# Kernel optimization log

Measured on AMD Instinct MI355X. Metric: run time of the kernel, lower is better.

The kernel has to match this reference:

```python
import jax, jax.numpy as jnp
import numpy as np

B, H, S, DH = 8, 16, 512, 64
HID = H * DH


def setup_inputs() -> dict:
    key = jax.random.key(0)
    ks = jax.random.split(key, 16)
    # padding vectors: 1s up to a per-sample valid length, 0s afterwards
    # (first zero index == valid length, matching create_padding_matrix semantics)
    len_q = jax.random.randint(ks[0], (B,), S // 2, S + 1)
    len_k = jax.random.randint(ks[1], (B,), S // 2, S + 1)
    r = jnp.arange(S)
    pq = (r[None, :] < len_q[:, None]).astype(jnp.int32)
    pk = (r[None, :] < len_k[:, None]).astype(jnp.int32)
    sc = 0.02
    inp = {
        "padding_vector_q": pq,
        "padding_vector_k": pk,
        "query_t_1": jnp.zeros((1,), jnp.float32),
        "key_t": jnp.zeros((1,), jnp.float32),
        "hidden_states": jnp.zeros((1,), jnp.float32),
        "hidden_states_t_1": jnp.zeros((1,), jnp.float32),
        "hidden_from_last": jax.random.normal(ks[2], (B, H, S, DH), jnp.float32),
        "hidden_current": jax.random.normal(ks[3], (B, H, S, DH), jnp.float32),
        "max_n_codes": S,
        "interpretabity": 0,
        "iter_idx": 0,
        "W_v1": jax.random.normal(ks[4], (HID, HID), jnp.float32) * sc,
        "b_v1": jnp.zeros((HID,), jnp.float32),
        "W_v": jax.random.normal(ks[5], (HID, HID), jnp.float32) * sc,
        "b_v": jnp.zeros((HID,), jnp.float32),
        "W_q": jax.random.normal(ks[6], (HID, HID), jnp.float32) * sc,
        "b_q": jnp.zeros((HID,), jnp.float32),
        "W_k": jax.random.normal(ks[7], (HID, HID), jnp.float32) * sc,
        "b_k": jnp.zeros((HID,), jnp.float32),
        "W_cat": jax.random.normal(ks[8], (2 * DH, DH), jnp.float32) * sc,
        "b_cat": jnp.zeros((DH,), jnp.float32),
    }
    return inp


def reference(padding_vector_q, padding_vector_k, query_t_1, key_t,
              hidden_states, hidden_states_t_1, hidden_from_last, hidden_current,
              max_n_codes, interpretabity, iter_idx,
              W_v1, b_v1, W_v, b_v, W_q, b_q, W_k, b_k, W_cat, b_cat):
    b, h, s, dh = hidden_from_last.shape
    hid = h * dh
    # permute(0,2,1,3).flatten(start_dim=2): [B,H,S,Dh] -> [B,S,H*Dh]
    flat_last = hidden_from_last.transpose(0, 2, 1, 3).reshape(b, s, hid)
    flat_cur = hidden_current.transpose(0, 2, 1, 3).reshape(b, s, hid)

    def heads(x):  # [B,S,HID] -> [B,H,S,Dh]
        return x.reshape(b, s, h, dh).transpose(0, 2, 1, 3)

    v1 = heads(flat_last @ W_v1 + b_v1)   # value_t_1(hidden_from_last)
    vt = heads(flat_cur @ W_v + b_v)      # value(hidden_current)
    q = heads(flat_last @ W_q + b_q)
    k = heads(flat_cur @ W_k + b_k)

    scores = jnp.einsum('bhqd,bhkd->bhqk', q, k) / jnp.sqrt(jnp.float32(dh))
    scores_t = scores.transpose(0, 1, 3, 2)  # [B,H,Sk,Sq] (original permute(0,1,3,2))

    # vectorized per-sample padding mask: valid window [0:padd_q, 0:padd_k]
    def first_zero(v):
        hz = jnp.any(v == 0, axis=1)
        return jnp.where(hz, jnp.argmax(v == 0, axis=1), s)

    pq_len = first_zero(padding_vector_q)
    pk_len = first_zero(padding_vector_k)
    r = jnp.arange(s)
    valid = (r[None, :, None] < pq_len[:, None, None]) & \
            (r[None, None, :] < pk_len[:, None, None])  # [B,S,S]
    mask = (~valid)[:, None, :, :]  # True = masked, broadcast over heads

    # -1e9 underflows to exactly 0 after softmax in fp32, matching the
    # masked_fill(-inf) -> softmax -> masked_fill(0) chain without NaN rows
    NEG = jnp.float32(-1e9)
    attn = jax.nn.softmax(jnp.where(mask, NEG, scores_t), axis=-1)
    attention_values = jnp.where(mask, jnp.float32(0), attn)

    context_layer = jnp.einsum('bhks,bhsd->bhkd', attention_values, v1)
    context_layer2 = jnp.concatenate([context_layer, vt], axis=-1) @ W_cat + b_cat
    return attention_values, scores_t, context_layer2, context_layer
```

## Files before the change

### kernel.cpp

```cpp
#include <hip/hip_runtime.h>
#include <cstddef>

#define NB 8
#define NH 16
#define NS 512
#define NDH 64
#define NHID 1024
#define NBH (NB*NH)

#define QKV_ELEMS (NB*NH*NS*NDH)
#define ATTN_ELEMS ((size_t)NB*NH*(size_t)NS*NS)

typedef __bf16 bf16;
typedef __attribute__((ext_vector_type(8))) __bf16 bf16x8;
typedef __attribute__((ext_vector_type(4))) __bf16 bf16x4;
typedef __attribute__((ext_vector_type(4))) float f32x4;
typedef unsigned int u32;

__device__ __forceinline__ void gload_lds16(const void* g, void* l) {
    __builtin_amdgcn_global_load_lds(
        (const __attribute__((address_space(1))) u32*)g,
        (__attribute__((address_space(3))) u32*)l, 16, 0, 0);
}

__device__ __forceinline__ int swz(int idx, int row) { return idx ^ ((row & 7) << 3); }

__global__ void lens_kernel(const int* __restrict__ pq, const int* __restrict__ pk,
                            int* __restrict__ lens) {
    int bi = blockIdx.x;
    const int* v = (bi < NB) ? pq : pk;
    int b = bi & (NB - 1);
    int lane = threadIdx.x;
    int local = NS;
#pragma unroll
    for (int p = 0; p < NS / 64; ++p) {
        int idx = p * 64 + lane;
        if (v[b * NS + idx] == 0 && idx < local) local = idx;
    }
#pragma unroll
    for (int m = 32; m >= 1; m >>= 1) {
        int o = __shfl_xor(local, m, 64);
        local = min(local, o);
    }
    if (lane == 0) lens[bi] = local;
}

__global__ __launch_bounds__(256) void cvtA_kernel(
    const float* __restrict__ hl, const float* __restrict__ hc,
    bf16* __restrict__ al, bf16* __restrict__ ac) {
    const float* src = blockIdx.z ? hc : hl;
    bf16* dst = blockIdx.z ? ac : al;
    int tid = blockIdx.x * 256 + threadIdx.x;
    int d8 = tid & 7, s = (tid >> 3) & 511, h = (tid >> 12) & 15, b = tid >> 16;
    const float* p = &src[(((size_t)b * NH + h) * NS + s) * NDH + d8 * 8];
    float4 v0 = *(const float4*)p;
    float4 v1 = *(const float4*)(p + 4);
    bf16x8 o;
    o[0] = (bf16)v0.x; o[1] = (bf16)v0.y; o[2] = (bf16)v0.z; o[3] = (bf16)v0.w;
    o[4] = (bf16)v1.x; o[5] = (bf16)v1.y; o[6] = (bf16)v1.z; o[7] = (bf16)v1.w;
    *(bf16x8*)&dst[((size_t)(b * NS + s)) * NHID + h * NDH + d8 * 8] = o;
}

__global__ __launch_bounds__(256) void cvtW_kernel(
    const float* __restrict__ Wq, const float* __restrict__ Wk,
    const float* __restrict__ Wv1, const float* __restrict__ Wv,
    bf16* __restrict__ Wt) {
    const float* W;
    switch (blockIdx.z) {
        case 0: W = Wq; break;
        case 1: W = Wk; break;
        case 2: W = Wv1; break;
        default: W = Wv; break;
    }
    bf16* out = Wt + (size_t)blockIdx.z * NHID * NHID;
    __shared__ bf16 T[64][72];
    int t = threadIdx.x;
    int k0 = blockIdx.y * 64, n0 = blockIdx.x * 64;
#pragma unroll
    for (int p = 0; p < 4; ++p) {
        int kk = p * 16 + (t >> 4), c4 = (t & 15) * 4;
        float4 v = *(const float4*)&W[(size_t)(k0 + kk) * NHID + n0 + c4];
        T[c4 + 0][kk] = (bf16)v.x;
        T[c4 + 1][kk] = (bf16)v.y;
        T[c4 + 2][kk] = (bf16)v.z;
        T[c4 + 3][kk] = (bf16)v.w;
    }
    __syncthreads();
#pragma unroll
    for (int p = 0; p < 2; ++p) {
        int f = p * 256 + t;
        int nn = f >> 3, k8 = (f & 7) * 8;
        bf16x8 o;
#pragma unroll
        for (int e = 0; e < 8; ++e) o[e] = T[nn][k8 + e];
        *(bf16x8*)&out[(size_t)(n0 + nn) * NHID + k0 + k8] = o;
    }
}

__global__ __launch_bounds__(256) void proj_kernel(
    const bf16* __restrict__ al, const bf16* __restrict__ ac,
    const bf16* __restrict__ Wt,
    const float* __restrict__ bq, const float* __restrict__ bk,
    const float* __restrict__ bv1, const float* __restrict__ bv,
    bf16* __restrict__ oq, bf16* __restrict__ ok,
    bf16* __restrict__ ov1, bf16* __restrict__ ovt) {
    __shared__ bf16 As[128 * 64];
    __shared__ bf16 Bs[128 * 64];
    const bf16* A; const bf16* W; const float* bias; bf16* dst;
    switch (blockIdx.z) {
        case 0: A = al; W = Wt;                 bias = bq;  dst = oq;  break;
        case 1: A = ac; W = Wt + 1048576;       bias = bk;  dst = ok;  break;
        case 2: A = al; W = Wt + 2097152;       bias = bv1; dst = ov1; break;
        default: A = ac; W = Wt + 3145728;      bias = bv;  dst = ovt; break;
    }
    int t = threadIdx.x, lane = t & 63, w = t >> 6;
    int wm = w & 1, wn = w >> 1;
    int m0 = blockIdx.y * 128, n0 = blockIdx.x * 128;
    int lrow = lane >> 3, lk8 = (lane & 7) * 8;
    f32x4 acc[4][4];
#pragma unroll
    for (int i = 0; i < 4; ++i)
#pragma unroll
        for (int j = 0; j < 4; ++j) acc[i][j] = (f32x4){0.f, 0.f, 0.f, 0.f};

    for (int kb = 0; kb < NHID; kb += 64) {
#pragma unroll
        for (int i = 0; i < 4; ++i) {
            int seg = w * 2048 + i * 512;
            int row = (w * 32 + i * 8) + lrow;
            gload_lds16(&A[(size_t)(m0 + row) * NHID + kb + lk8], &As[seg]);
            gload_lds16(&W[(size_t)(n0 + row) * NHID + kb + lk8], &Bs[seg]);
        }
        __syncthreads();
#pragma unroll
        for (int ks = 0; ks < 2; ++ks) {
            int ko = ks * 32 + (lane >> 4) * 8;
            bf16x8 a[4], bb[4];
#pragma unroll
            for (int i = 0; i < 4; ++i)
                a[i] = *(const bf16x8*)&As[(wm * 64 + i * 16 + (lane & 15)) * 64 + ko];
#pragma unroll
            for (int j = 0; j < 4; ++j)
                bb[j] = *(const bf16x8*)&Bs[(wn * 64 + j * 16 + (lane & 15)) * 64 + ko];
#pragma unroll
            for (int i = 0; i < 4; ++i)
#pragma unroll
                for (int j = 0; j < 4; ++j)
                    acc[i][j] = __builtin_amdgcn_mfma_f32_16x16x32_bf16(a[i], bb[j], acc[i][j], 0, 0, 0);
        }
        __syncthreads();
    }
    float bsv[4];
#pragma unroll
    for (int j = 0; j < 4; ++j) bsv[j] = bias[n0 + wn * 64 + j * 16 + (lane & 15)];
#pragma unroll
    for (int i = 0; i < 4; ++i)
#pragma unroll
        for (int r = 0; r < 4; ++r) {
            int m = m0 + wm * 64 + i * 16 + (lane >> 4) * 4 + r;
            int b = m >> 9, s = m & (NS - 1);
#pragma unroll
            for (int j = 0; j < 4; ++j) {
                int n = n0 + wn * 64 + j * 16 + (lane & 15);
                dst[(((size_t)b * NH + (n >> 6)) * NS + s) * NDH + (n & 63)] =
                    (bf16)(acc[i][j][r] + bsv[j]);
            }
        }
}

__global__ __launch_bounds__(256) void attn_fused_kernel(
    const bf16* __restrict__ qb, const bf16* __restrict__ kb,
    const bf16* __restrict__ v1, const int* __restrict__ lens,
    float* __restrict__ scores, float* __restrict__ attn,
    float* __restrict__ ctx) {
    __shared__ bf16 Ks[64 * 64];
    __shared__ bf16 Ps[64 * 128];
    __shared__ bf16 Vs[64 * 128];
    __shared__ float redm[4][64];
    __shared__ float reds[4][64];
    int bh = blockIdx.y, ki0 = blockIdx.x * 64;
    int b = bh >> 4;
    int t = threadIdx.x, lane = t & 63, w = t >> 6;
    int lq = lens[b], lk = lens[NB + b];
    const bf16* kbb = kb + ((size_t)bh * NS + ki0) * NDH;
    const bf16* qbb = qb + (size_t)bh * NS * NDH;
    const bf16* vb  = v1 + (size_t)bh * NS * NDH;
#pragma unroll
    for (int p = 0; p < 2; ++p) {
        int f = p * 256 + t;
        int row = f >> 3, d8 = (f & 7) * 8;
        bf16x8 v = *(const bf16x8*)&kbb[(size_t)row * NDH + d8];
        *(bf16x8*)&Ks[swz(row * 64 + d8, row)] = v;
    }
    __syncthreads();
    f32x4 acc[4][8];
#pragma unroll
    for (int i = 0; i < 4; ++i)
#pragma unroll
        for (int j = 0; j < 8; ++j) acc[i][j] = (f32x4){0.f, 0.f, 0.f, 0.f};
#pragma unroll
    for (int ds = 0; ds < 2; ++ds) {
        int kofs = ds * 32 + (lane >> 4) * 8;
        bf16x8 a[4];
#pragma unroll
        for (int i = 0; i < 4; ++i) {
            int row = i * 16 + (lane & 15);
            a[i] = *(const bf16x8*)&Ks[swz(row * 64 + kofs, row)];
        }
#pragma unroll
        for (int j = 0; j < 8; ++j) {
            int qi = w * 128 + j * 16 + (lane & 15);
            bf16x8 bq8 = *(const bf16x8*)&qbb[(size_t)qi * NDH + kofs];
#pragma unroll
            for (int i = 0; i < 4; ++i)
                acc[i][j] = __builtin_amdgcn_mfma_f32_16x16x32_bf16(a[i], bq8, acc[i][j], 0, 0, 0);
        }
    }
    int g = lane >> 4, c = lane & 15;
    float pmax[4][4];
#pragma unroll
    for (int i = 0; i < 4; ++i)
#pragma unroll
        for (int r = 0; r < 4; ++r) pmax[i][r] = -3.0e38f;
#pragma unroll
    for (int i = 0; i < 4; ++i)
#pragma unroll
        for (int j = 0; j < 8; ++j) {
            int qi = w * 128 + j * 16 + c;
            bool colv = qi < lk;
#pragma unroll
            for (int r = 0; r < 4; ++r) {
                float s = acc[i][j][r] * 0.125f;
                acc[i][j][r] = s;
                scores[((size_t)bh * NS + ki0 + i * 16 + g * 4 + r) * NS + qi] = s;
                if (colv) pmax[i][r] = fmaxf(pmax[i][r], s);
            }
        }
#pragma unroll
    for (int msk = 8; msk >= 1; msk >>= 1)
#pragma unroll
        for (int i = 0; i < 4; ++i)
#pragma unroll
            for (int r = 0; r < 4; ++r)
                pmax[i][r] = fmaxf(pmax[i][r], __shfl_xor(pmax[i][r], msk, 64));
    if (c == 0)
#pragma unroll
        for (int i = 0; i < 4; ++i)
#pragma unroll
            for (int r = 0; r < 4; ++r) redm[w][i * 16 + g * 4 + r] = pmax[i][r];
    __syncthreads();
    float rmax[4][4];
#pragma unroll
    for (int i = 0; i < 4; ++i)
#pragma unroll
        for (int r = 0; r < 4; ++r) {
            int row = i * 16 + g * 4 + r;
            rmax[i][r] = fmaxf(fmaxf(redm[0][row], redm[1][row]),
                               fmaxf(redm[2][row], redm[3][row]));
        }
    float psum[4][4];
#pragma unroll
    for (int i = 0; i < 4; ++i)
#pragma unroll
        for (int r = 0; r < 4; ++r) psum[i][r] = 0.f;
#pragma unroll
    for (int i = 0; i < 4; ++i)
#pragma unroll
        for (int j = 0; j < 8; ++j) {
            int qi = w * 128 + j * 16 + c;
            bool colv = qi < lk;
#pragma unroll
            for (int r = 0; r < 4; ++r) {
                float e = colv ? __expf(acc[i][j][r] - rmax[i][r]) : 0.f;
                acc[i][j][r] = e;
                psum[i][r] += e;
            }
        }
#pragma unroll
    for (int msk = 8; msk >= 1; msk >>= 1)
#pragma unroll
        for (int i = 0; i < 4; ++i)
#pragma unroll
            for (int r = 0; r < 4; ++r)
                psum[i][r] += __shfl_xor(psum[i][r], msk, 64);
    if (c == 0)
#pragma unroll
        for (int i = 0; i < 4; ++i)
#pragma unroll
            for (int r = 0; r < 4; ++r) reds[w][i * 16 + g * 4 + r] = psum[i][r];
    __syncthreads();
#pragma unroll
    for (int i = 0; i < 4; ++i)
#pragma unroll
        for (int r = 0; r < 4; ++r) {
            int row = i * 16 + g * 4 + r;
            float rs = reds[0][row] + reds[1][row] + reds[2][row] + reds[3][row];
            float inv = (rs > 0.f) ? 1.f / rs : 0.f;
            bool rowv = (ki0 + row) < lq;
            float fin = rowv ? inv : 0.f;
#pragma unroll
            for (int j = 0; j < 8; ++j) {
                int qi = w * 128 + j * 16 + c;
                float v = acc[i][j][r] * fin;
                acc[i][j][r] = v;
                attn[((size_t)bh * NS + ki0 + row) * NS + qi] = v;
            }
        }
    if (ki0 >= lq) {
#pragma unroll
        for (int p = 0; p < 4; ++p) {
            int f = p * 256 + t;
            int row = f >> 4, c4 = (f & 15) * 4;
            *(float4*)&ctx[((size_t)bh * NS + ki0 + row) * NDH + c4] =
                make_float4(0.f, 0.f, 0.f, 0.f);
        }
        return;
    }
    f32x4 cacc[4];
#pragma unroll
    for (int j = 0; j < 4; ++j) cacc[j] = (f32x4){0.f, 0.f, 0.f, 0.f};
    for (int cq = 0; cq < 4; ++cq) {
        if (cq * 128 >= lk) break;
        __syncthreads();
#pragma unroll
        for (int p = 0; p < 4; ++p) {
            int f = p * 256 + t;
            int qr = f >> 3, d8 = (f & 7) * 8;
            bf16x8 v = *(const bf16x8*)&vb[(size_t)(cq * 128 + qr) * NDH + d8];
#pragma unroll
            for (int e = 0; e < 8; ++e)
                Vs[swz((d8 + e) * 128 + qr, d8 + e)] = v[e];
        }
        if (w == cq) {
#pragma unroll
            for (int i = 0; i < 4; ++i)
#pragma unroll
                for (int j = 0; j < 8; ++j) {
                    int qc = j * 16 + c;
#pragma unroll
                    for (int r = 0; r < 4; ++r) {
                        int row = i * 16 + g * 4 + r;
                        Ps[swz(row * 128 + qc, row)] = (bf16)acc[i][j][r];
                    }
                }
        }
        __syncthreads();
#pragma unroll
        for (int ks = 0; ks < 4; ++ks) {
            int kofs = ks * 32 + (lane >> 4) * 8;
            int arow = w * 16 + (lane & 15);
            bf16x8 a = *(const bf16x8*)&Ps[swz(arow * 128 + kofs, arow)];
#pragma unroll
            for (int j = 0; j < 4; ++j) {
                int d = j * 16 + (lane & 15);
                bf16x8 bv8 = *(const bf16x8*)&Vs[swz(d * 128 + kofs, d)];
                cacc[j] = __builtin_amdgcn_mfma_f32_16x16x32_bf16(a, bv8, cacc[j], 0, 0, 0);
            }
        }
    }
#pragma unroll
    for (int j = 0; j < 4; ++j)
#pragma unroll
        for (int r = 0; r < 4; ++r) {
            int ki = ki0 + w * 16 + g * 4 + r;
            ctx[((size_t)bh * NS + ki) * NDH + j * 16 + c] = cacc[j][r];
        }
}

__global__ __launch_bounds__(256) void cat_kernel(
    const float* __restrict__ ctx, const bf16* __restrict__ vt,
    const float* __restrict__ Wcat, const float* __restrict__ bcat,
    float* __restrict__ out) {
    __shared__ float As[16][68];
    __shared__ float Bs[16][68];
    int t = threadIdx.x;
    int tx = t & 15, ty = t >> 4;
    int row0 = blockIdx.x * 64;
    float acc[4][4];
#pragma unroll
    for (int i = 0; i < 4; ++i)
#pragma unroll
        for (int j = 0; j < 4; ++j) acc[i][j] = 0.f;

    for (int k0 = 0; k0 < 2 * NDH; k0 += 16) {
#pragma unroll
        for (int p = 0; p < 4; ++p) {
            int e = p * 256 + t;
            int kk = e & 15, mm = e >> 4;
            int cidx = k0 + kk;
            float val = (cidx < NDH) ? ctx[(size_t)(row0 + mm) * NDH + cidx]
                                     : (float)vt[(size_t)(row0 + mm) * NDH + (cidx - NDH)];
            As[kk][mm] = val;
        }
#pragma unroll
        for (int p = 0; p < 4; ++p) {
            int e = p * 256 + t;
            int nn = e & 63, kk = e >> 6;
            Bs[kk][nn] = Wcat[(size_t)(k0 + kk) * NDH + nn];
        }
        __syncthreads();
#pragma unroll
        for (int kk = 0; kk < 16; ++kk) {
            float a[4], bb[4];
            *(float4*)&a[0]  = *(const float4*)&As[kk][ty * 4];
            *(float4*)&bb[0] = *(const float4*)&Bs[kk][tx * 4];
#pragma unroll
            for (int i = 0; i < 4; ++i)
#pragma unroll
                for (int j = 0; j < 4; ++j) acc[i][j] += a[i] * bb[j];
        }
        __syncthreads();
    }
#pragma unroll
    for (int i = 0; i < 4; ++i) {
        int n = tx * 4;
        float4 o;
        o.x = acc[i][0] + bcat[n + 0];
        o.y = acc[i][1] + bcat[n + 1];
        o.z = acc[i][2] + bcat[n + 2];
        o.w = acc[i][3] + bcat[n + 3];
        *(float4*)&out[(size_t)(row0 + ty * 4 + i) * NDH + n] = o;
    }
}

extern "C" void kernel_launch(void* const* d_in, const int* in_sizes, int n_in,
                              void* d_out, int out_size, void* d_ws, size_t ws_size,
                              hipStream_t stream) {
    (void)in_sizes; (void)n_in; (void)out_size; (void)ws_size;
    const int*   pq   = (const int*)d_in[0];
    const int*   pk   = (const int*)d_in[1];
    const float* hl   = (const float*)d_in[6];
    const float* hc   = (const float*)d_in[7];
    const float* Wv1  = (const float*)d_in[11];
    const float* bv1  = (const float*)d_in[12];
    const float* Wv   = (const float*)d_in[13];
    const float* bv   = (const float*)d_in[14];
    const float* Wq   = (const float*)d_in[15];
    const float* bq   = (const float*)d_in[16];
    const float* Wk   = (const float*)d_in[17];
    const float* bk   = (const float*)d_in[18];
    const float* Wcat = (const float*)d_in[19];
    const float* bcat = (const float*)d_in[20];

    float* out_attn   = (float*)d_out;
    float* out_scores = out_attn + ATTN_ELEMS;
    float* out_ctx2   = out_attn + 2 * ATTN_ELEMS;
    float* out_ctx    = out_ctx2 + QKV_ELEMS;

    char* ws = (char*)d_ws;
    bf16* al   = (bf16*)(ws);
    bf16* acb  = (bf16*)(ws + 8388608);
    bf16* WtB  = (bf16*)(ws + 16777216);
    bf16* qb   = (bf16*)(ws + 25165824);
    bf16* kbp  = (bf16*)(ws + 33554432);
    bf16* v1b  = (bf16*)(ws + 41943040);
    bf16* vtb  = (bf16*)(ws + 50331648);
    int*  lens = (int*)(ws + 58720256);

    lens_kernel<<<16, 64, 0, stream>>>(pq, pk, lens);
    cvtA_kernel<<<dim3(2048, 1, 2), 256, 0, stream>>>(hl, hc, al, acb);
    cvtW_kernel<<<dim3(16, 16, 4), 256, 0, stream>>>(Wq, Wk, Wv1, Wv, WtB);
    proj_kernel<<<dim3(8, 32, 4), 256, 0, stream>>>(
        al, acb, WtB, bq, bk, bv1, bv, qb, kbp, v1b, vtb);
    attn_fused_kernel<<<dim3(8, NBH), 256, 0, stream>>>(
        qb, kbp, v1b, lens, out_scores, out_attn, out_ctx);
    cat_kernel<<<(NB * NH * NS) / 64, 256, 0, stream>>>(out_ctx, vtb, Wcat, bcat, out_ctx2);
}
```

Baseline: 495.9 us.

## Halve attention key tile to 32 rows, stage full P row in LDS

The fused attention kernel now handles 32 key rows per block instead of 64, which doubles the grid to 16 blocks per batch-head and shrinks per-thread accumulator registers. Normalized probabilities for the whole 512-wide row are written to LDS once, so the per-chunk writes of P by a single wave are gone, and the PV product is re-partitioned so each wave owns 16 head dims. Fully masked key tiles now exit early and write zeros for attn and ctx. It also adds s_setprio hints around the MFMA loops. The trade-off is more blocks re-reading Q and V from global memory, plus a larger LDS footprint for Ps.

Result: faster. 484.0 us (-2.4%).

```diff
diff --git a/kernel.cpp b/kernel.cpp
--- a/kernel.cpp
+++ b/kernel.cpp
@@ -173,57 +173,58 @@
     const bf16* __restrict__ v1, const int* __restrict__ lens,
     float* __restrict__ scores, float* __restrict__ attn,
     float* __restrict__ ctx) {
-    __shared__ bf16 Ks[64 * 64];
-    __shared__ bf16 Ps[64 * 128];
+    __shared__ bf16 Ks[32 * 64];
+    __shared__ bf16 Ps[32 * 512];
     __shared__ bf16 Vs[64 * 128];
-    __shared__ float redm[4][64];
-    __shared__ float reds[4][64];
-    int bh = blockIdx.y, ki0 = blockIdx.x * 64;
+    __shared__ float redm[4][32];
+    __shared__ float reds[4][32];
+    int bh = blockIdx.y, ki0 = blockIdx.x * 32;
     int b = bh >> 4;
     int t = threadIdx.x, lane = t & 63, w = t >> 6;
     int lq = lens[b], lk = lens[NB + b];
     const bf16* kbb = kb + ((size_t)bh * NS + ki0) * NDH;
     const bf16* qbb = qb + (size_t)bh * NS * NDH;
     const bf16* vb  = v1 + (size_t)bh * NS * NDH;
-#pragma unroll
-    for (int p = 0; p < 2; ++p) {
-        int f = p * 256 + t;
-        int row = f >> 3, d8 = (f & 7) * 8;
+    {
+        int row = t >> 3, d8 = (t & 7) * 8;
         bf16x8 v = *(const bf16x8*)&kbb[(size_t)row * NDH + d8];
         *(bf16x8*)&Ks[swz(row * 64 + d8, row)] = v;
     }
     __syncthreads();
-    f32x4 acc[4][8];
-#pragma unroll
-    for (int i = 0; i < 4; ++i)
+    f32x4 acc[2][8];
+#pragma unroll
+    for (int i = 0; i < 2; ++i)
 #pragma unroll
         for (int j = 0; j < 8; ++j) acc[i][j] = (f32x4){0.f, 0.f, 0.f, 0.f};
 #pragma unroll
     for (int ds = 0; ds < 2; ++ds) {
         int kofs = ds * 32 + (lane >> 4) * 8;
-        bf16x8 a[4];
-#pragma unroll
-        for (int i = 0; i < 4; ++i) {
+        bf16x8 a[2];
+#pragma unroll
+        for (int i = 0; i < 2; ++i) {
             int row = i * 16 + (lane & 15);
             a[i] = *(const bf16x8*)&Ks[swz(row * 64 + kofs, row)];
         }
+        __builtin_amdgcn_s_setprio(1);
 #pragma unroll
         for (int j = 0; j < 8; ++j) {
             int qi = w * 128 + j * 16 + (lane & 15);
             bf16x8 bq8 = *(const bf16x8*)&qbb[(size_t)qi * NDH + kofs];
 #pragma unroll
-            for (int i = 0; i < 4; ++i)
+            for (int i = 0; i < 2; ++i)
                 acc[i][j] = __builtin_amdgcn_mfma_f32_16x16x32_bf16(a[i], bq8, acc[i][j], 0, 0, 0);
         }
+        __builtin_amdgcn_s_setprio(0);
     }
     int g = lane >> 4, c = lane & 15;
-    float pmax[4][4];
-#pragma unroll
-    for (int i = 0; i < 4; ++i)
+    bool fullmask = (ki0 >= lq);
+    float pmax[2][4];
+#pragma unroll
+    for (int i = 0; i < 2; ++i)
 #pragma unroll
         for (int r = 0; r < 4; ++r) pmax[i][r] = -3.0e38f;
 #pragma unroll
-    for (int i = 0; i < 4; ++i)
+    for (int i = 0; i < 2; ++i)
 #pragma unroll
         for (int j = 0; j < 8; ++j) {
             int qi = w * 128 + j * 16 + c;
@@ -236,35 +237,47 @@
                 if (colv) pmax[i][r] = fmaxf(pmax[i][r], s);
             }
         }
+    if (fullmask) {
+        float* ab = attn + ((size_t)bh * NS + ki0) * NS;
+        float4 z = make_float4(0.f, 0.f, 0.f, 0.f);
+#pragma unroll
+        for (int p = 0; p < 16; ++p)
+            *(float4*)&ab[(p * 256 + t) * 4] = z;
+        float* cb = ctx + ((size_t)bh * NS + ki0) * NDH;
+#pragma unroll
+        for (int p = 0; p < 2; ++p)
+            *(float4*)&cb[(p * 256 + t) * 4] = z;
+        return;
+    }
 #pragma unroll
     for (int msk = 8; msk >= 1; msk >>= 1)
 #pragma unroll
-        for (int i = 0; i < 4; ++i)
+        for (int i = 0; i < 2; ++i)
 #pragma unroll
             for (int r = 0; r < 4; ++r)
                 pmax[i][r] = fmaxf(pmax[i][r], __shfl_xor(pmax[i][r], msk, 64));
     if (c == 0)
 #pragma unroll
-        for (int i = 0; i < 4; ++i)
+        for (int i = 0; i < 2; ++i)
 #pragma unroll
             for (int r = 0; r < 4; ++r) redm[w][i * 16 + g * 4 + r] = pmax[i][r];
     __syncthreads();
-    float rmax[4][4];
-#pragma unroll
-    for (int i = 0; i < 4; ++i)
+    float rmax[2][4];
+#pragma unroll
+    for (int i = 0; i < 2; ++i)
 #pragma unroll
         for (int r = 0; r < 4; ++r) {
             int row = i * 16 + g * 4 + r;
             rmax[i][r] = fmaxf(fmaxf(redm[0][row], redm[1][row]),
                                fmaxf(redm[2][row], redm[3][row]));
         }
-    float psum[4][4];
-#pragma unroll
-    for (int i = 0; i < 4; ++i)
+    float psum[2][4];
+#pragma unroll
+    for (int i = 0; i < 2; ++i)
 #pragma unroll
         for (int r = 0; r < 4; ++r) psum[i][r] = 0.f;
 #pragma unroll
-    for (int i = 0; i < 4; ++i)
+    for (int i = 0; i < 2; ++i)
 #pragma unroll
         for (int j = 0; j < 8; ++j) {
             int qi = w * 128 + j * 16 + c;
@@ -279,18 +292,18 @@
 #pragma unroll
     for (int msk = 8; msk >= 1; msk >>= 1)
 #pragma unroll
-        for (int i = 0; i < 4; ++i)
+        for (int i = 0; i < 2; ++i)
 #pragma unroll
             for (int r = 0; r < 4; ++r)
                 psum[i][r] += __shfl_xor(psum[i][r], msk, 64);
     if (c == 0)
 #pragma unroll
-        for (int i = 0; i < 4; ++i)
+        for (int i = 0; i < 2; ++i)
 #pragma unroll
             for (int r = 0; r < 4; ++r) reds[w][i * 16 + g * 4 + r] = psum[i][r];
     __syncthreads();
 #pragma unroll
-    for (int i = 0; i < 4; ++i)
+    for (int i = 0; i < 2; ++i)
 #pragma unroll
         for (int r = 0; r < 4; ++r) {
             int row = i * 16 + g * 4 + r;
@@ -304,21 +317,12 @@
                 float v = acc[i][j][r] * fin;
                 acc[i][j][r] = v;
                 attn[((size_t)bh * NS + ki0 + row) * NS + qi] = v;
+                Ps[swz(row * 512 + qi, row)] = (bf16)v;
             }
         }
-    if (ki0 >= lq) {
-#pragma unroll
-        for (int p = 0; p < 4; ++p) {
-            int f = p * 256 + t;
-            int row = f >> 4, c4 = (f & 15) * 4;
-            *(float4*)&ctx[((size_t)bh * NS + ki0 + row) * NDH + c4] =
-                make_float4(0.f, 0.f, 0.f, 0.f);
-        }
-        return;
-    }
-    f32x4 cacc[4];
-#pragma unroll
-    for (int j = 0; j < 4; ++j) cacc[j] = (f32x4){0.f, 0.f, 0.f, 0.f};
+    f32x4 cacc[2];
+#pragma unroll
+    for (int i = 0; i < 2; ++i) cacc[i] = (f32x4){0.f, 0.f, 0.f, 0.f};
     for (int cq = 0; cq < 4; ++cq) {
         if (cq * 128 >= lk) break;
         __syncthreads();
@@ -331,39 +335,28 @@
             for (int e = 0; e < 8; ++e)
                 Vs[swz((d8 + e) * 128 + qr, d8 + e)] = v[e];
         }
-        if (w == cq) {
-#pragma unroll
-            for (int i = 0; i < 4; ++i)
-#pragma unroll
-                for (int j = 0; j < 8; ++j) {
-                    int qc = j * 16 + c;
-#pragma unroll
-                    for (int r = 0; r < 4; ++r) {
-                        int row = i * 16 + g * 4 + r;
-                        Ps[swz(row * 128 + qc, row)] = (bf16)acc[i][j][r];
-                    }
-                }
-        }
-        __syncthreads();
+        __syncthreads();
+        __builtin_amdgcn_s_setprio(1);
 #pragma unroll
         for (int ks = 0; ks < 4; ++ks) {
-            int kofs = ks * 32 + (lane >> 4) * 8;
-            int arow = w * 16 + (lane & 15);
-            bf16x8 a = *(const bf16x8*)&Ps[swz(arow * 128 + kofs, arow)];
-#pragma unroll
-            for (int j = 0; j < 4; ++j) {
-                int d = j * 16 + (lane & 15);
-                bf16x8 bv8 = *(const bf16x8*)&Vs[swz(d * 128 + kofs, d)];
-                cacc[j] = __builtin_amdgcn_mfma_f32_16x16x32_bf16(a, bv8, cacc[j], 0, 0, 0);
+            int klo = ks * 32 + (lane >> 4) * 8;
+            int d = w * 16 + (lane & 15);
+            bf16x8 bv8 = *(const bf16x8*)&Vs[swz(d * 128 + klo, d)];
+#pragma unroll
+            for (int i = 0; i < 2; ++i) {
+                int arow = i * 16 + (lane & 15);
+                bf16x8 pa = *(const bf16x8*)&Ps[swz(arow * 512 + cq * 128 + klo, arow)];
+                cacc[i] = __builtin_amdgcn_mfma_f32_16x16x32_bf16(pa, bv8, cacc[i], 0, 0, 0);
             }
         }
-    }
-#pragma unroll
-    for (int j = 0; j < 4; ++j)
+        __builtin_amdgcn_s_setprio(0);
+    }
+#pragma unroll
+    for (int i = 0; i < 2; ++i)
 #pragma unroll
         for (int r = 0; r < 4; ++r) {
-            int ki = ki0 + w * 16 + g * 4 + r;
-            ctx[((size_t)bh * NS + ki) * NDH + j * 16 + c] = cacc[j][r];
+            int ki = ki0 + i * 16 + g * 4 + r;
+            ctx[((size_t)bh * NS + ki) * NDH + w * 16 + c] = cacc[i][r];
         }
 }
 
@@ -462,7 +455,7 @@
     cvtW_kernel<<<dim3(16, 16, 4), 256, 0, stream>>>(Wq, Wk, Wv1, Wv, WtB);
     proj_kernel<<<dim3(8, 32, 4), 256, 0, stream>>>(
         al, acb, WtB, bq, bk, bv1, bv, qb, kbp, v1b, vtb);
-    attn_fused_kernel<<<dim3(8, NBH), 256, 0, stream>>>(
+    attn_fused_kernel<<<dim3(16, NBH), 256, 0, stream>>>(
         qb, kbp, v1b, lens, out_scores, out_attn, out_ctx);
     cat_kernel<<<(NB * NH * NS) / 64, 256, 0, stream>>>(out_ctx, vtb, Wcat, bcat, out_ctx2);
 }
```
